# Kernel optimization log

Measured on AMD Instinct MI355X. Metric: run time of the kernel, lower is better.

Reference implementation:

```python
import math
import jax, jax.numpy as jnp
import numpy as np

B, N, C = 64, 197, 768
H = 12
D = C // H
SCALE = D ** -0.5
EPS_SM = 1e-6
LN_EPS = 1e-5


def _layernorm(x, w, b):
    mu = jnp.mean(x, axis=-1, keepdims=True)
    var = jnp.var(x, axis=-1, keepdims=True)
    return (x - mu) * jax.lax.rsqrt(var + LN_EPS) * w + b


def setup_inputs() -> dict:
    key = jax.random.key(0)
    ks = jax.random.split(key, 12)
    s = 0.02
    return {
        "x": jax.random.normal(ks[0], (B, N, C), jnp.float32),
        "mask": jnp.ones((B, N), jnp.float32),
        "ln1_w": jnp.ones((C,), jnp.float32),
        "ln1_b": jnp.zeros((C,), jnp.float32),
        "qkv_w": jax.random.normal(ks[1], (C, 3 * C), jnp.float32) * s,
        "qkv_b": jnp.zeros((3 * C,), jnp.float32),
        "proj_w": jax.random.normal(ks[2], (C, C), jnp.float32) * s,
        "proj_b": jnp.zeros((C,), jnp.float32),
        "ln2_w": jnp.ones((C,), jnp.float32),
        "ln2_b": jnp.zeros((C,), jnp.float32),
        "fc1_w": jax.random.normal(ks[3], (C, 4 * C), jnp.float32) * s,
        "fc1_b": jnp.zeros((4 * C,), jnp.float32),
        "fc2_w": jax.random.normal(ks[4], (4 * C, C), jnp.float32) * s,
        "fc2_b": jnp.zeros((C,), jnp.float32),
        "threshold": jnp.float32(0.0),
    }


def reference(x, mask, ln1_w, ln1_b, qkv_w, qkv_b, proj_w, proj_b,
              ln2_w, ln2_b, fc1_w, fc1_b, fc2_w, fc2_b, threshold):
    # --- LTPAttention ---
    h = _layernorm(x, ln1_w, ln1_b)
    qkv = (h @ qkv_w + qkv_b).reshape(B, N, 3, H, D)
    qkv = jnp.transpose(qkv, (2, 0, 3, 1, 4))  # (3, B, H, N, D)
    q, k, v = qkv[0], qkv[1], qkv[2]
    attn = jnp.einsum("bhnd,bhmd->bhnm", q, k) * SCALE  # (B,H,N,N)
    # softmax_with_mask (eval path): exp * key-mask, renormalize
    m = mask[:, None, None, :]  # (B,1,1,N) masks keys
    w = jnp.exp(attn - jnp.max(attn, axis=-1, keepdims=True)) * m
    attn = w / (jnp.sum(w, axis=-1, keepdims=True) + EPS_SM)
    out = jnp.einsum("bhnm,bhmd->bhnd", attn, v)
    out = jnp.transpose(out, (0, 2, 1, 3)).reshape(B, N, C)
    x_attn = out @ proj_w + proj_b
    # importance scores: mean over heads and queries -> (B, N)
    imp = jnp.mean(attn, axis=(1, 2))
    imp = imp.at[:, 0].set(jnp.inf)  # always keep CLS token
    # ThresholdMasker (eval): hard threshold
    new_mask = (imp > threshold).astype(mask.dtype)
    mask_out = jnp.where(mask > 0, new_mask, mask)
    # --- residual + MLP ---
    x = x + x_attn
    h2 = _layernorm(x, ln2_w, ln2_b)
    h2 = jax.nn.gelu(h2 @ fc1_w + fc1_b, approximate=False)
    x = x + (h2 @ fc2_w + fc2_b)
    return x, mask_out
```

## Files before the change

### kernel.cpp

```cpp
#include <hip/hip_runtime.h>
#include <hip/hip_bf16.h>
#include <math.h>

#define B_ 64
#define N_ 197
#define C_ 768
#define H_ 12
#define BN_ (B_ * N_)
#define MPAD 12672
#define GRIDM 99

typedef unsigned short ushort_t;
typedef __attribute__((ext_vector_type(8))) short short8;
typedef __attribute__((ext_vector_type(4))) float f32x4;

__device__ __forceinline__ float wave_reduce_sum(float v) {
#pragma unroll
  for (int off = 32; off; off >>= 1) v += __shfl_xor(v, off);
  return v;
}

__device__ __forceinline__ ushort_t f2bf(float f) {
  __hip_bfloat16 h = __float2bfloat16(f);
  ushort_t u;
  __builtin_memcpy(&u, &h, 2);
  return u;
}

__device__ __forceinline__ float gelu_fast(float u) {
  const float z2 = 1.5957691216f * (u + 0.044715f * u * u * u);
  const float e = __expf(z2);
  const float th = 1.f - 2.f / (e + 1.f);
  return 0.5f * u * (1.f + th);
}

__global__ __launch_bounds__(256) void wtrans_kernel(const float* __restrict__ W,
                                                     ushort_t* __restrict__ Wt,
                                                     int K, int N) {
  __shared__ ushort_t tile[32][33];
  const int bn = blockIdx.x * 32, bk = blockIdx.y * 32;
  const int tx = threadIdx.x & 31, ty = threadIdx.x >> 5;
#pragma unroll
  for (int i = ty; i < 32; i += 8)
    tile[i][tx] = f2bf(W[(size_t)(bk + i) * N + bn + tx]);
  __syncthreads();
#pragma unroll
  for (int i = ty; i < 32; i += 8)
    Wt[(size_t)(bn + i) * K + bk + tx] = tile[tx][i];
}

__global__ __launch_bounds__(256) void ln_kernel(const float* __restrict__ x,
                                                 const float* __restrict__ w,
                                                 const float* __restrict__ bsh,
                                                 ushort_t* __restrict__ out) {
  const int row = blockIdx.x;
  const float* xr = x + (size_t)row * C_;
  const int tid = threadIdx.x;
  float v0 = xr[tid], v1 = xr[tid + 256], v2 = xr[tid + 512];
  float s = v0 + v1 + v2;
  float q = v0 * v0 + v1 * v1 + v2 * v2;
  s = wave_reduce_sum(s);
  q = wave_reduce_sum(q);
  __shared__ float red[8];
  const int w4 = tid >> 6, l = tid & 63;
  if (l == 0) { red[w4] = s; red[4 + w4] = q; }
  __syncthreads();
  float ts = red[0] + red[1] + red[2] + red[3];
  float tq = red[4] + red[5] + red[6] + red[7];
  float mu = ts * (1.f / C_);
  float var = tq * (1.f / C_) - mu * mu;
  float rs = rsqrtf(var + 1e-5f);
  ushort_t* orow = out + (size_t)row * C_;
  orow[tid]       = f2bf((v0 - mu) * rs * w[tid]       + bsh[tid]);
  orow[tid + 256] = f2bf((v1 - mu) * rs * w[tid + 256] + bsh[tid + 256]);
  orow[tid + 512] = f2bf((v2 - mu) * rs * w[tid + 512] + bsh[tid + 512]);
}

template <int RES, int ACT, int OUT_BF16>
__global__ __launch_bounds__(256) void mfma_gemm(const ushort_t* __restrict__ A,
                                                 const ushort_t* __restrict__ Bt,
                                                 const float* __restrict__ bias,
                                                 const float* __restrict__ res,
                                                 void* __restrict__ Cout,
                                                 int M, int Nc, int K, int gridN) {
  __shared__ __align__(16) ushort_t As0[128][32];
  __shared__ __align__(16) ushort_t As1[128][32];
  __shared__ __align__(16) ushort_t As2[128][32];
  __shared__ __align__(16) ushort_t Bs0[128][32];
  __shared__ __align__(16) ushort_t Bs1[128][32];
  __shared__ __align__(16) ushort_t Bs2[128][32];

  const int flat = blockIdx.x;
  const int x8 = flat & 7, q8 = flat >> 3;
  const int n_t = q8 % gridN, jj = q8 / gridN;
  const int m_t = jj * 8 + x8;
  if (m_t >= GRIDM) return;

  const int tid = threadIdx.x;
  const int w = tid >> 6, l = tid & 63;
  const int bm = m_t * 128, bnn = n_t * 128;
  const int quad = l >> 4, lm = l & 15;
  const int wm = (w >> 1) * 64, wn = (w & 1) * 64;

  const int c0 = w * 2, c1 = w * 2 + 1;
  const int srow = l >> 2;
  const int scol = ((l & 3) ^ ((l >> 3) & 3)) << 3;
  const ushort_t* ag0 = A + (size_t)(bm + c0 * 16 + srow) * K + scol;
  const ushort_t* ag1 = A + (size_t)(bm + c1 * 16 + srow) * K + scol;
  const ushort_t* bg0 = Bt + (size_t)(bnn + c0 * 16 + srow) * K + scol;
  const ushort_t* bg1 = Bt + (size_t)(bnn + c1 * 16 + srow) * K + scol;

  auto stage = [&](ushort_t (*Ad)[32], ushort_t (*Bd)[32], int k0) {
    __builtin_amdgcn_global_load_lds(
        (const __attribute__((address_space(1))) void*)(ag0 + k0),
        (__attribute__((address_space(3))) void*)&Ad[c0 * 16][0], 16, 0, 0);
    __builtin_amdgcn_global_load_lds(
        (const __attribute__((address_space(1))) void*)(ag1 + k0),
        (__attribute__((address_space(3))) void*)&Ad[c1 * 16][0], 16, 0, 0);
    __builtin_amdgcn_global_load_lds(
        (const __attribute__((address_space(1))) void*)(bg0 + k0),
        (__attribute__((address_space(3))) void*)&Bd[c0 * 16][0], 16, 0, 0);
    __builtin_amdgcn_global_load_lds(
        (const __attribute__((address_space(1))) void*)(bg1 + k0),
        (__attribute__((address_space(3))) void*)&Bd[c1 * 16][0], 16, 0, 0);
  };

  const int fslot = (quad ^ ((lm >> 1) & 3)) << 3;

  f32x4 acc[4][4];
#pragma unroll
  for (int mi = 0; mi < 4; mi++)
#pragma unroll
    for (int ni = 0; ni < 4; ni++) acc[mi][ni] = (f32x4){0.f, 0.f, 0.f, 0.f};

  const int NIT = K >> 5;

#define GSTEP(Ac, Bc, An, Bn, tn, VMN, DOSTAGE)                             \
  {                                                                         \
    asm volatile("s_waitcnt vmcnt(" #VMN ") lgkmcnt(0)" ::: "memory");      \
    __builtin_amdgcn_s_barrier();                                           \
    asm volatile("" ::: "memory");                                          \
    if (DOSTAGE) stage(An, Bn, (tn) << 5);                                  \
    short8 af[4], bf[4];                                                    \
    _Pragma("unroll") for (int i = 0; i < 4; i++) {                         \
      af[i] = *(const short8*)&Ac[wm + i * 16 + lm][fslot];                 \
      bf[i] = *(const short8*)&Bc[wn + i * 16 + lm][fslot];                 \
    }                                                                       \
    _Pragma("unroll") for (int mi = 0; mi < 4; mi++)                        \
      _Pragma("unroll") for (int ni = 0; ni < 4; ni++)                      \
        acc[mi][ni] = __builtin_amdgcn_mfma_f32_16x16x32_bf16(              \
            af[mi], bf[ni], acc[mi][ni], 0, 0, 0);                          \
  }

  stage(As0, Bs0, 0);
  stage(As1, Bs1, 1 << 5);
  int t = 0;
  for (; t < NIT - 3; t += 3) {
    GSTEP(As0, Bs0, As2, Bs2, t + 2, 4, true);
    GSTEP(As1, Bs1, As0, Bs0, t + 3, 4, true);
    GSTEP(As2, Bs2, As1, Bs1, t + 4, 4, true);
  }
  GSTEP(As0, Bs0, As2, Bs2, t + 2, 4, true);
  GSTEP(As1, Bs1, As0, Bs0, 0, 4, false);
  GSTEP(As2, Bs2, As0, Bs0, 0, 0, false);
#undef GSTEP

#pragma unroll
  for (int mi = 0; mi < 4; mi++) {
#pragma unroll
    for (int ni = 0; ni < 4; ni++) {
      const int col = bnn + wn + ni * 16 + lm;
      const float bv = bias[col];
#pragma unroll
      for (int r = 0; r < 4; r++) {
        const int row = bm + wm + mi * 16 + quad * 4 + r;
        if (row < M) {
          float v = acc[mi][ni][r] + bv;
          if constexpr (RES) v += res[(size_t)row * Nc + col];
          if constexpr (ACT) v = gelu_fast(v);
          if constexpr (OUT_BF16)
            ((ushort_t*)Cout)[(size_t)row * Nc + col] = f2bf(v);
          else
            ((float*)Cout)[(size_t)row * Nc + col] = v;
        }
      }
    }
  }
}

__global__ __launch_bounds__(256, 2) void attn_mfma(const ushort_t* __restrict__ qkv,
                                                    const float* __restrict__ mask,
                                                    ushort_t* __restrict__ aout,
                                                    float* __restrict__ imp) {
  __shared__ __align__(16) ushort_t Ks[208 * 64];
  __shared__ __align__(16) ushort_t Vt[64 * 216];
  __shared__ __align__(16) ushort_t Pb[4][16 * 208];
  const int b = blockIdx.x / H_, h = blockIdx.x % H_;
  const int tid = threadIdx.x, w = tid >> 6, l = tid & 63;
  const int quad = l >> 4, lm = l & 15;
  const ushort_t* qbase = qkv + (size_t)b * N_ * 2304 + h * 64;
  const ushort_t* kbase = qbase + 768;
  const ushort_t* vbase = qbase + 1536;

  for (int idx = tid; idx < 208 * 8; idx += 256) {
    const int j = idx >> 3, g = idx & 7;
    uint4 val = make_uint4(0u, 0u, 0u, 0u);
    if (j < N_) val = *(const uint4*)(kbase + (size_t)j * 2304 + g * 8);
    *(uint4*)&Ks[j * 64 + ((g ^ (j & 7)) << 3)] = val;
  }
  for (int idx = tid; idx < 52 * 64; idx += 256) {
    const int d = idx & 63, jg = idx >> 6, j0 = jg * 4;
    ushort_t a0 = 0, a1 = 0, a2 = 0, a3 = 0;
    if (j0 + 0 < N_) a0 = vbase[(size_t)(j0 + 0) * 2304 + d];
    if (j0 + 1 < N_) a1 = vbase[(size_t)(j0 + 1) * 2304 + d];
    if (j0 + 2 < N_) a2 = vbase[(size_t)(j0 + 2) * 2304 + d];
    if (j0 + 3 < N_) a3 = vbase[(size_t)(j0 + 3) * 2304 + d];
    uint2 pk;
    pk.x = (unsigned)a0 | ((unsigned)a1 << 16);
    pk.y = (unsigned)a2 | ((unsigned)a3 << 16);
    *(uint2*)&Vt[d * 216 + j0] = pk;
  }
  float mkv[13];
#pragma unroll
  for (int t = 0; t < 13; t++) {
    const int col = t * 16 + lm;
    mkv[t] = (col < N_) ? mask[b * N_ + col] : 0.f;
  }
  float cs[13];
#pragma unroll
  for (int t = 0; t < 13; t++) cs[t] = 0.f;
  __syncthreads();

  ushort_t* pw = &Pb[w][0];
  for (int i0 = w * 16; i0 < 208; i0 += 64) {
    f32x4 accs[13];
#pragma unroll
    for (int t = 0; t < 13; t++) accs[t] = (f32x4){0.f, 0.f, 0.f, 0.f};
#pragma unroll
    for (int kh = 0; kh < 2; kh++) {
      const int k0 = kh * 32;
      const short8 aq =
          *(const short8*)(qbase + (size_t)(i0 + lm) * 2304 + k0 + quad * 8);
      const int gb = (k0 >> 3) + quad;
#pragma unroll
      for (int t = 0; t < 13; t++) {
        const int j = t * 16 + lm;
        const short8 bk = *(const short8*)&Ks[j * 64 + ((gb ^ (j & 7)) << 3)];
        accs[t] = __builtin_amdgcn_mfma_f32_16x16x32_bf16(aq, bk, accs[t], 0, 0, 0);
      }
    }
    float inv[4];
#pragma unroll
    for (int r = 0; r < 4; r++) {
      float m = -3.4e38f;
#pragma unroll
      for (int t = 0; t < 13; t++) m = fmaxf(m, accs[t][r] * 0.125f);
      m = fmaxf(m, __shfl_xor(m, 1));
      m = fmaxf(m, __shfl_xor(m, 2));
      m = fmaxf(m, __shfl_xor(m, 4));
      m = fmaxf(m, __shfl_xor(m, 8));
      float s = 0.f;
#pragma unroll
      for (int t = 0; t < 13; t++) {
        const float e = __expf(accs[t][r] * 0.125f - m) * mkv[t];
        accs[t][r] = e;
        s += e;
      }
      s += __shfl_xor(s, 1);
      s += __shfl_xor(s, 2);
      s += __shfl_xor(s, 4);
      s += __shfl_xor(s, 8);
      inv[r] = 1.f / (s + 1e-6f);
    }
    const int ibase = i0 + quad * 4;
#pragma unroll
    for (int r = 0; r < 4; r++) {
      const bool rok = (ibase + r) < N_;
#pragma unroll
      for (int t = 0; t < 13; t++) {
        const float p = accs[t][r] * inv[r];
        accs[t][r] = p;
        if (rok) cs[t] += p;
        pw[(quad * 4 + r) * 208 + t * 16 + lm] = f2bf(p);
      }
    }
    __builtin_amdgcn_wave_barrier();
    f32x4 acco[4];
#pragma unroll
    for (int n = 0; n < 4; n++) acco[n] = (f32x4){0.f, 0.f, 0.f, 0.f};
#pragma unroll
    for (int ks = 0; ks < 6; ks++) {
      const int k0 = ks * 32;
      const short8 ap = *(const short8*)&pw[lm * 208 + k0 + quad * 8];
#pragma unroll
      for (int n = 0; n < 4; n++) {
        const short8 bv = *(const short8*)&Vt[(n * 16 + lm) * 216 + k0 + quad * 8];
        acco[n] = __builtin_amdgcn_mfma_f32_16x16x32_bf16(ap, bv, acco[n], 0, 0, 0);
      }
    }
    {
      const bool lo = (quad < 2);
      short8 apt = {};
      if (lo) apt = *(const short8*)&pw[lm * 208 + 192 + quad * 8];
#pragma unroll
      for (int n = 0; n < 4; n++) {
        short8 bvt = {};
        if (lo) bvt = *(const short8*)&Vt[(n * 16 + lm) * 216 + 192 + quad * 8];
        acco[n] = __builtin_amdgcn_mfma_f32_16x16x32_bf16(apt, bvt, acco[n], 0, 0, 0);
      }
    }
#pragma unroll
    for (int r = 0; r < 4; r++) {
      const int i = ibase + r;
      if (i < N_) {
#pragma unroll
        for (int n = 0; n < 4; n++)
          aout[(size_t)(b * N_ + i) * C_ + h * 64 + n * 16 + lm] = f2bf(acco[n][r]);
      }
    }
  }
#pragma unroll
  for (int t = 0; t < 13; t++) {
    float v = cs[t];
    v += __shfl_xor(v, 16);
    v += __shfl_xor(v, 32);
    if (l < 16) {
      const int col = t * 16 + l;
      if (col < N_)
        atomicAdd(&imp[b * N_ + col], v * (1.f / (H_ * (float)N_)));
    }
  }
}

__global__ __launch_bounds__(256) void mask_kernel(const float* __restrict__ imp,
                                                   const float* __restrict__ mask,
                                                   const float* __restrict__ thr,
                                                   float* __restrict__ mask_out) {
  const int i = blockIdx.x * 256 + threadIdx.x;
  if (i >= BN_) return;
  const int n = i % N_;
  const float iv = (n == 0) ? INFINITY : imp[i];
  const float m = mask[i];
  const float nm = (iv > thr[0]) ? 1.f : 0.f;
  mask_out[i] = (m > 0.f) ? nm : m;
}

extern "C" void kernel_launch(void* const* d_in, const int* in_sizes, int n_in,
                              void* d_out, int out_size, void* d_ws, size_t ws_size,
                              hipStream_t stream) {
  const float* x      = (const float*)d_in[0];
  const float* mask   = (const float*)d_in[1];
  const float* ln1_w  = (const float*)d_in[2];
  const float* ln1_b  = (const float*)d_in[3];
  const float* qkv_w  = (const float*)d_in[4];
  const float* qkv_b  = (const float*)d_in[5];
  const float* proj_w = (const float*)d_in[6];
  const float* proj_b = (const float*)d_in[7];
  const float* ln2_w  = (const float*)d_in[8];
  const float* ln2_b  = (const float*)d_in[9];
  const float* fc1_w  = (const float*)d_in[10];
  const float* fc1_b  = (const float*)d_in[11];
  const float* fc2_w  = (const float*)d_in[12];
  const float* fc2_b  = (const float*)d_in[13];
  const float* thr    = (const float*)d_in[14];

  float* out = (float*)d_out;
  float* mask_out = out + (size_t)BN_ * C_;

  ushort_t* buf0    = (ushort_t*)d_ws;
  ushort_t* hbuf    = buf0 + (size_t)MPAD * 3072;
  ushort_t* aoutb   = hbuf + (size_t)MPAD * 768;
  ushort_t* qkv_wt  = aoutb + (size_t)MPAD * 768;
  ushort_t* proj_wt = qkv_wt + (size_t)2304 * 768;
  ushort_t* fc1_wt  = proj_wt + (size_t)768 * 768;
  ushort_t* fc2_wt  = fc1_wt + (size_t)3072 * 768;
  float*    impb    = (float*)(fc2_wt + (size_t)768 * 3072);

  hipMemsetAsync(impb, 0, BN_ * sizeof(float), stream);

  wtrans_kernel<<<dim3(2304 / 32, 768 / 32), 256, 0, stream>>>(qkv_w, qkv_wt, 768, 2304);
  wtrans_kernel<<<dim3(768 / 32, 768 / 32), 256, 0, stream>>>(proj_w, proj_wt, 768, 768);
  wtrans_kernel<<<dim3(3072 / 32, 768 / 32), 256, 0, stream>>>(fc1_w, fc1_wt, 768, 3072);
  wtrans_kernel<<<dim3(768 / 32, 3072 / 32), 256, 0, stream>>>(fc2_w, fc2_wt, 3072, 768);

  const int MS = 13 * 8;
  ln_kernel<<<BN_, 256, 0, stream>>>(x, ln1_w, ln1_b, hbuf);
  mfma_gemm<0, 0, 1><<<MS * 18, 256, 0, stream>>>(
      hbuf, qkv_wt, qkv_b, nullptr, buf0, BN_, 2304, 768, 18);
  attn_mfma<<<B_ * H_, 256, 0, stream>>>(buf0, mask, aoutb, impb);
  mask_kernel<<<(BN_ + 255) / 256, 256, 0, stream>>>(impb, mask, thr, mask_out);
  mfma_gemm<1, 0, 0><<<MS * 6, 256, 0, stream>>>(
      aoutb, proj_wt, proj_b, x, out, BN_, 768, 768, 6);
  ln_kernel<<<BN_, 256, 0, stream>>>(out, ln2_w, ln2_b, hbuf);
  mfma_gemm<0, 1, 1><<<MS * 24, 256, 0, stream>>>(
      hbuf, fc1_wt, fc1_b, nullptr, buf0, BN_, 3072, 768, 24);
  mfma_gemm<1, 0, 0><<<MS * 6, 256, 0, stream>>>(
      buf0, fc2_wt, fc2_b, out, out, BN_, 768, 3072, 6);
}
```

Before: 614.4 us.

## Enlarge GEMM tile to 256x128 with 8 waves and raise MFMA priority

The GEMM block grows from 128x128 with 4 waves to 256x128 with 8 waves, and the padded row count and M grid shrink to match. Each wave now stages three 16B loads instead of four, and the wait count moves from 4 to 3. Each B tile is reused across twice as many A rows, which cuts global/L2 traffic per FLOP. s_setprio is also raised around the MFMA loop. The cost is more LDS per block, fewer blocks in the grid (possible wave quantization on the 256 CUs), and more row padding waste at 12800 rows.

Measured after the change: 653.9 us. 1.06x slower.

```diff
diff --git a/kernel.cpp b/kernel.cpp
--- a/kernel.cpp
+++ b/kernel.cpp
@@ -7,8 +7,8 @@
 #define C_ 768
 #define H_ 12
 #define BN_ (B_ * N_)
-#define MPAD 12672
-#define GRIDM 99
+#define RPAD 12800
+#define GRIDM2 50
 
 typedef unsigned short ushort_t;
 typedef __attribute__((ext_vector_type(8))) short short8;
@@ -77,15 +77,15 @@
 }
 
 template <int RES, int ACT, int OUT_BF16>
-__global__ __launch_bounds__(256) void mfma_gemm(const ushort_t* __restrict__ A,
+__global__ __launch_bounds__(512) void mfma_gemm(const ushort_t* __restrict__ A,
                                                  const ushort_t* __restrict__ Bt,
                                                  const float* __restrict__ bias,
                                                  const float* __restrict__ res,
                                                  void* __restrict__ Cout,
                                                  int M, int Nc, int K, int gridN) {
-  __shared__ __align__(16) ushort_t As0[128][32];
-  __shared__ __align__(16) ushort_t As1[128][32];
-  __shared__ __align__(16) ushort_t As2[128][32];
+  __shared__ __align__(16) ushort_t As0[256][32];
+  __shared__ __align__(16) ushort_t As1[256][32];
+  __shared__ __align__(16) ushort_t As2[256][32];
   __shared__ __align__(16) ushort_t Bs0[128][32];
   __shared__ __align__(16) ushort_t Bs1[128][32];
   __shared__ __align__(16) ushort_t Bs2[128][32];
@@ -94,35 +94,30 @@
   const int x8 = flat & 7, q8 = flat >> 3;
   const int n_t = q8 % gridN, jj = q8 / gridN;
   const int m_t = jj * 8 + x8;
-  if (m_t >= GRIDM) return;
+  if (m_t >= GRIDM2) return;
 
   const int tid = threadIdx.x;
   const int w = tid >> 6, l = tid & 63;
-  const int bm = m_t * 128, bnn = n_t * 128;
+  const int bm = m_t * 256, bnn = n_t * 128;
   const int quad = l >> 4, lm = l & 15;
   const int wm = (w >> 1) * 64, wn = (w & 1) * 64;
 
-  const int c0 = w * 2, c1 = w * 2 + 1;
   const int srow = l >> 2;
   const int scol = ((l & 3) ^ ((l >> 3) & 3)) << 3;
-  const ushort_t* ag0 = A + (size_t)(bm + c0 * 16 + srow) * K + scol;
-  const ushort_t* ag1 = A + (size_t)(bm + c1 * 16 + srow) * K + scol;
-  const ushort_t* bg0 = Bt + (size_t)(bnn + c0 * 16 + srow) * K + scol;
-  const ushort_t* bg1 = Bt + (size_t)(bnn + c1 * 16 + srow) * K + scol;
+  const ushort_t* ag0 = A + (size_t)(bm + w * 32 + srow) * K + scol;
+  const ushort_t* ag1 = A + (size_t)(bm + w * 32 + 16 + srow) * K + scol;
+  const ushort_t* bg0 = Bt + (size_t)(bnn + w * 16 + srow) * K + scol;
 
   auto stage = [&](ushort_t (*Ad)[32], ushort_t (*Bd)[32], int k0) {
     __builtin_amdgcn_global_load_lds(
         (const __attribute__((address_space(1))) void*)(ag0 + k0),
-        (__attribute__((address_space(3))) void*)&Ad[c0 * 16][0], 16, 0, 0);
+        (__attribute__((address_space(3))) void*)&Ad[w * 32][0], 16, 0, 0);
     __builtin_amdgcn_global_load_lds(
         (const __attribute__((address_space(1))) void*)(ag1 + k0),
-        (__attribute__((address_space(3))) void*)&Ad[c1 * 16][0], 16, 0, 0);
+        (__attribute__((address_space(3))) void*)&Ad[w * 32 + 16][0], 16, 0, 0);
     __builtin_amdgcn_global_load_lds(
         (const __attribute__((address_space(1))) void*)(bg0 + k0),
-        (__attribute__((address_space(3))) void*)&Bd[c0 * 16][0], 16, 0, 0);
-    __builtin_amdgcn_global_load_lds(
-        (const __attribute__((address_space(1))) void*)(bg1 + k0),
-        (__attribute__((address_space(3))) void*)&Bd[c1 * 16][0], 16, 0, 0);
+        (__attribute__((address_space(3))) void*)&Bd[w * 16][0], 16, 0, 0);
   };
 
   const int fslot = (quad ^ ((lm >> 1) & 3)) << 3;
@@ -146,22 +141,24 @@
       af[i] = *(const short8*)&Ac[wm + i * 16 + lm][fslot];                 \
       bf[i] = *(const short8*)&Bc[wn + i * 16 + lm][fslot];                 \
     }                                                                       \
+    __builtin_amdgcn_s_setprio(1);                                          \
     _Pragma("unroll") for (int mi = 0; mi < 4; mi++)                        \
       _Pragma("unroll") for (int ni = 0; ni < 4; ni++)                      \
         acc[mi][ni] = __builtin_amdgcn_mfma_f32_16x16x32_bf16(              \
             af[mi], bf[ni], acc[mi][ni], 0, 0, 0);                          \
+    __builtin_amdgcn_s_setprio(0);                                          \
   }
 
   stage(As0, Bs0, 0);
   stage(As1, Bs1, 1 << 5);
   int t = 0;
   for (; t < NIT - 3; t += 3) {
-    GSTEP(As0, Bs0, As2, Bs2, t + 2, 4, true);
-    GSTEP(As1, Bs1, As0, Bs0, t + 3, 4, true);
-    GSTEP(As2, Bs2, As1, Bs1, t + 4, 4, true);
-  }
-  GSTEP(As0, Bs0, As2, Bs2, t + 2, 4, true);
-  GSTEP(As1, Bs1, As0, Bs0, 0, 4, false);
+    GSTEP(As0, Bs0, As2, Bs2, t + 2, 3, true);
+    GSTEP(As1, Bs1, As0, Bs0, t + 3, 3, true);
+    GSTEP(As2, Bs2, As1, Bs1, t + 4, 3, true);
+  }
+  GSTEP(As0, Bs0, As2, Bs2, t + 2, 3, true);
+  GSTEP(As1, Bs1, As0, Bs0, 0, 3, false);
   GSTEP(As2, Bs2, As0, Bs0, 0, 0, false);
 #undef GSTEP
 
@@ -368,9 +365,9 @@
   float* mask_out = out + (size_t)BN_ * C_;
 
   ushort_t* buf0    = (ushort_t*)d_ws;
-  ushort_t* hbuf    = buf0 + (size_t)MPAD * 3072;
-  ushort_t* aoutb   = hbuf + (size_t)MPAD * 768;
-  ushort_t* qkv_wt  = aoutb + (size_t)MPAD * 768;
+  ushort_t* hbuf    = buf0 + (size_t)RPAD * 3072;
+  ushort_t* aoutb   = hbuf + (size_t)RPAD * 768;
+  ushort_t* qkv_wt  = aoutb + (size_t)RPAD * 768;
   ushort_t* proj_wt = qkv_wt + (size_t)2304 * 768;
   ushort_t* fc1_wt  = proj_wt + (size_t)768 * 768;
   ushort_t* fc2_wt  = fc1_wt + (size_t)3072 * 768;
@@ -383,17 +380,17 @@
   wtrans_kernel<<<dim3(3072 / 32, 768 / 32), 256, 0, stream>>>(fc1_w, fc1_wt, 768, 3072);
   wtrans_kernel<<<dim3(768 / 32, 3072 / 32), 256, 0, stream>>>(fc2_w, fc2_wt, 3072, 768);
 
-  const int MS = 13 * 8;
+  const int MS = 7 * 8;
   ln_kernel<<<BN_, 256, 0, stream>>>(x, ln1_w, ln1_b, hbuf);
-  mfma_gemm<0, 0, 1><<<MS * 18, 256, 0, stream>>>(
+  mfma_gemm<0, 0, 1><<<MS * 18, 512, 0, stream>>>(
       hbuf, qkv_wt, qkv_b, nullptr, buf0, BN_, 2304, 768, 18);
   attn_mfma<<<B_ * H_, 256, 0, stream>>>(buf0, mask, aoutb, impb);
   mask_kernel<<<(BN_ + 255) / 256, 256, 0, stream>>>(impb, mask, thr, mask_out);
-  mfma_gemm<1, 0, 0><<<MS * 6, 256, 0, stream>>>(
+  mfma_gemm<1, 0, 0><<<MS * 6, 512, 0, stream>>>(
       aoutb, proj_wt, proj_b, x, out, BN_, 768, 768, 6);
   ln_kernel<<<BN_, 256, 0, stream>>>(out, ln2_w, ln2_b, hbuf);
-  mfma_gemm<0, 1, 1><<<MS * 24, 256, 0, stream>>>(
+  mfma_gemm<0, 1, 1><<<MS * 24, 512, 0, stream>>>(
       hbuf, fc1_wt, fc1_b, nullptr, buf0, BN_, 3072, 768, 24);
-  mfma_gemm<1, 0, 0><<<MS * 6, 256, 0, stream>>>(
+  mfma_gemm<1, 0, 0><<<MS * 6, 512, 0, stream>>>(
       buf0, fc2_wt, fc2_b, out, out, BN_, 768, 3072, 6);
 }
```
